# Kernel optimization log

Measured on AMD Instinct MI355X. Metric: run time of the kernel, lower is better.

Reference implementation:

```python
import jax, jax.numpy as jnp
import numpy as np

N_NODES = 50000
N_EDGES = 800000
IN_FEATS = 128
H_FEATS = 32
HEADS = 4
OUT_FEATS = 32
OUT_HEADS = 1
NEG_SLOPE = 0.2


def setup_inputs() -> dict:
    key = jax.random.key(0)
    ks = jax.random.split(key, 20)
    s = 0.05
    return {
        "features": jax.random.normal(ks[0], (N_NODES, IN_FEATS), jnp.float32),
        "src": jax.random.randint(ks[1], (N_EDGES,), 0, N_NODES, jnp.int32),
        "dst": jax.random.randint(ks[2], (N_EDGES,), 0, N_NODES, jnp.int32),
        "Ws0": jax.random.normal(ks[3], (IN_FEATS, HEADS * H_FEATS), jnp.float32) * s,
        "bs0": jnp.zeros((HEADS * H_FEATS,), jnp.float32),
        "Wd0": jax.random.normal(ks[4], (IN_FEATS, HEADS * H_FEATS), jnp.float32) * s,
        "bd0": jnp.zeros((HEADS * H_FEATS,), jnp.float32),
        "a0": jax.random.normal(ks[5], (HEADS, H_FEATS), jnp.float32) * s,
        "Ws1": jax.random.normal(ks[6], (HEADS * H_FEATS, HEADS * H_FEATS), jnp.float32) * s,
        "bs1": jnp.zeros((HEADS * H_FEATS,), jnp.float32),
        "Wd1": jax.random.normal(ks[7], (HEADS * H_FEATS, HEADS * H_FEATS), jnp.float32) * s,
        "bd1": jnp.zeros((HEADS * H_FEATS,), jnp.float32),
        "a1": jax.random.normal(ks[8], (HEADS, H_FEATS), jnp.float32) * s,
        "Ws2": jax.random.normal(ks[9], (HEADS * H_FEATS, OUT_HEADS * OUT_FEATS), jnp.float32) * s,
        "bs2": jnp.zeros((OUT_HEADS * OUT_FEATS,), jnp.float32),
        "Wd2": jax.random.normal(ks[10], (HEADS * H_FEATS, OUT_HEADS * OUT_FEATS), jnp.float32) * s,
        "bd2": jnp.zeros((OUT_HEADS * OUT_FEATS,), jnp.float32),
        "a2": jax.random.normal(ks[11], (OUT_HEADS, OUT_FEATS), jnp.float32) * s,
    }


def gatv2_conv(x, src, dst, Ws, bs, Wd, bd, attn, n_nodes):
    """DGL GATv2Conv (share_weights=False, residual=False, no dropout)."""
    heads, f = attn.shape
    feat_src = (x @ Ws + bs).reshape(-1, heads, f)  # [N, H, F]
    feat_dst = (x @ Wd + bd).reshape(-1, heads, f)  # [N, H, F]
    # per-edge GATv2 score: LeakyReLU(Wsrc h_u + Wdst h_v) . a
    e = jax.nn.leaky_relu(feat_src[src] + feat_dst[dst], NEG_SLOPE)  # [E, H, F]
    logits = jnp.einsum("ehf,hf->eh", e, attn)  # [E, H]
    # edge softmax over incoming edges of each dst node
    m = jax.ops.segment_max(logits, dst, num_segments=n_nodes)  # [N, H]
    ex = jnp.exp(logits - m[dst])
    denom = jax.ops.segment_sum(ex, dst, num_segments=n_nodes)  # [N, H]
    alpha = ex / denom[dst]  # [E, H]
    # scatter-aggregate messages
    msg = feat_src[src] * alpha[..., None]  # [E, H, F]
    return jax.ops.segment_sum(msg, dst, num_segments=n_nodes)  # [N, H, F]


def reference(features, src, dst,
              Ws0, bs0, Wd0, bd0, a0,
              Ws1, bs1, Wd1, bd1, a1,
              Ws2, bs2, Wd2, bd2, a2):
    n = features.shape[0]
    h = gatv2_conv(features, src, dst, Ws0, bs0, Wd0, bd0, a0, n)
    h = jax.nn.relu(h.reshape(n, -1))
    h = gatv2_conv(h, src, dst, Ws1, bs1, Wd1, bd1, a1, n)
    h = jax.nn.relu(h.reshape(n, -1))
    h = gatv2_conv(h, src, dst, Ws2, bs2, Wd2, bd2, a2, n)
    return h.mean(axis=1)  # [N, OUT_FEATS]
```

## Files before the change

### kernel.cpp

```cpp
#include <hip/hip_runtime.h>

typedef __attribute__((ext_vector_type(8))) short bf16x8;
typedef __attribute__((ext_vector_type(4))) float f32x4;

#define LOG2E 1.4426950408889634f

#define BINSH 8
#define NBIN 196
#define CHUNK 4096
#define K4CAP 6144

__device__ __forceinline__ unsigned bf_rn(float f) {
    unsigned u = __float_as_uint(f);
    u += 0x7fffu + ((u >> 16) & 1u);
    return u >> 16;
}
__device__ __forceinline__ float bf_lo(unsigned u) { return __uint_as_float(u << 16); }
__device__ __forceinline__ float bf_hi(unsigned u) { return __uint_as_float(u & 0xffff0000u); }

template <int CTRL>
__device__ __forceinline__ float dpp_radd(float x) {
    int t = __builtin_amdgcn_update_dpp(0, __float_as_int(x), CTRL, 0xF, 0xF, true);
    return x + __int_as_float(t);
}
__device__ __forceinline__ float sum8(float p) {
    p = dpp_radd<0x141>(p);
    p = dpp_radd<0x1B>(p);
    p = dpp_radd<0xB1>(p);
    return p;
}
__device__ __forceinline__ float dpp_swap1(float x) {
    return __int_as_float(__builtin_amdgcn_update_dpp(0, __float_as_int(x), 0xB1, 0xF, 0xF, true));
}

__device__ __forceinline__ float fast_exp2(float x) {
#if __has_builtin(__builtin_amdgcn_exp2f)
    return __builtin_amdgcn_exp2f(x);
#else
    return __expf(x * 0.6931471805599453f);
#endif
}


__global__ __launch_bounds__(256) void prep(
    const float* __restrict__ x, unsigned short* __restrict__ xb, int n4,
    const float* __restrict__ Ws0, const float* __restrict__ Wd0,
    const float* __restrict__ Ws1, const float* __restrict__ Wd1,
    const float* __restrict__ Ws2, const float* __restrict__ Wd2,
    unsigned short* __restrict__ wt0, unsigned short* __restrict__ wt1,
    unsigned short* __restrict__ wt2, int* __restrict__ binCnt,
    int* __restrict__ binOff) {
    int gid = blockIdx.x * blockDim.x + threadIdx.x;
    if (gid < NBIN) { binCnt[gid] = 0; binOff[gid] = 0; }
    if (gid < n4) {
        float4 v = *(const float4*)(x + (size_t)gid * 4);
        ushort4 r;
        r.x = (unsigned short)bf_rn(v.x); r.y = (unsigned short)bf_rn(v.y);
        r.z = (unsigned short)bf_rn(v.z); r.w = (unsigned short)bf_rn(v.w);
        *(ushort4*)(xb + (size_t)gid * 4) = r;
    } else {
        int g = gid - n4;
        if (g < 65536) {
            int l = g >> 15, loc = g & 32767;
            int c = loc >> 7, k = loc & 127;
            const float* W = (c < 128) ? (l ? Ws1 : Ws0) : (l ? Wd1 : Wd0);
            int cc = c & 127;
            float v = W[(size_t)k * 128 + cc];
            (l ? wt1 : wt0)[loc] = (unsigned short)bf_rn(v);
        } else if (g < 65536 + 8192) {
            int loc = g - 65536;
            int c = loc >> 7, k = loc & 127;
            const float* W = (c < 32) ? Ws2 : Wd2;
            int cc = (c < 32) ? c : c - 32;
            float v = W[(size_t)k * 32 + cc];
            wt2[loc] = (unsigned short)bf_rn(v);
        }
    }
}


template <int COLS2>
__device__ __forceinline__ void gemm_core(
    const unsigned short* __restrict__ xb, const unsigned short* __restrict__ wt,
    const float* __restrict__ bs, const float* __restrict__ bd,
    unsigned short* __restrict__ fs, unsigned short* __restrict__ fd,
    int n, int nch, int gwid, int nwaves) {
    constexpr int C  = COLS2 / 2;
    constexpr int NC = COLS2 / 64;

    const int lane = threadIdx.x & 63;
    const int m = lane & 15, quad = lane >> 4;
    const int cs = gwid % NC;
    const int cstride = nwaves / NC;

    float biasv[4];
#pragma unroll
    for (int ct = 0; ct < 4; ++ct) {
        int col = cs * 64 + ct * 16 + m;
        biasv[ct] = (col < C) ? bs[col] : bd[col - C];
    }

    for (int chunk = gwid / NC; chunk < nch; chunk += cstride) {
        const size_t r0 = (size_t)chunk * 64;

        f32x4 acc[4][4];
#pragma unroll
        for (int rt = 0; rt < 4; ++rt)
#pragma unroll
            for (int ct = 0; ct < 4; ++ct) acc[rt][ct] = (f32x4){0.f, 0.f, 0.f, 0.f};

#pragma unroll
        for (int ks = 0; ks < 4; ++ks) {
            const int ko = ks * 32 + quad * 8;
            bf16x8 a[4], b[4];
#pragma unroll
            for (int rt = 0; rt < 4; ++rt)
                a[rt] = *(const bf16x8*)(xb + (r0 + rt * 16 + m) * 128 + ko);
#pragma unroll
            for (int ct = 0; ct < 4; ++ct)
                b[ct] = *(const bf16x8*)(wt + (size_t)(cs * 64 + ct * 16 + m) * 128 + ko);
#pragma unroll
            for (int rt = 0; rt < 4; ++rt)
#pragma unroll
                for (int ct = 0; ct < 4; ++ct)
                    acc[rt][ct] = __builtin_amdgcn_mfma_f32_16x16x32_bf16(a[rt], b[ct], acc[rt][ct], 0, 0, 0);
        }

        const int odd = m & 1;
#pragma unroll
        for (int ct = 0; ct < 4; ++ct) {
            int colE = cs * 64 + ct * 16 + (m & ~1);
            unsigned short* ptr = (colE < C) ? fs : fd;
            int cc = (colE < C) ? colE : colE - C;
#pragma unroll
            for (int rt = 0; rt < 4; ++rt) {
                float v0 = acc[rt][ct][0] + biasv[ct];
                float v1 = acc[rt][ct][1] + biasv[ct];
                float v2 = acc[rt][ct][2] + biasv[ct];
                float v3 = acc[rt][ct][3] + biasv[ct];
                float s0 = dpp_swap1(v0), s1 = dpp_swap1(v1);
                float s2 = dpp_swap1(v2), s3 = dpp_swap1(v3);
                float aLo = odd ? s2 : v0, aHi = odd ? v2 : s0;
                float bLo = odd ? s3 : v1, bHi = odd ? v3 : s1;
                int rowA = (int)r0 + rt * 16 + quad * 4 + (odd ? 2 : 0);
                unsigned pa = (bf_rn(aHi) << 16) | bf_rn(aLo);
                unsigned pb = (bf_rn(bHi) << 16) | bf_rn(bLo);
                if (rowA < n)     *(unsigned*)(ptr + (size_t)rowA * C + cc)       = pa;
                if (rowA + 1 < n) *(unsigned*)(ptr + ((size_t)rowA + 1) * C + cc) = pb;
            }
        }
    }
}

template <int COLS2>
__global__ __launch_bounds__(256) void gemm_dual2(
    const unsigned short* __restrict__ xb, const unsigned short* __restrict__ wt,
    const float* __restrict__ bs, const float* __restrict__ bd,
    unsigned short* __restrict__ fs, unsigned short* __restrict__ fd,
    int n, int nch) {
    gemm_core<COLS2>(xb, wt, bs, bd, fs, fd, n, nch,
                     blockIdx.x * 4 + (threadIdx.x >> 6), gridDim.x * 4);
}


__global__ __launch_bounds__(256) void count_gemm0(
    const int* __restrict__ dst, int* __restrict__ binCnt, int e, int nchunks,
    const unsigned short* __restrict__ xb, const unsigned short* __restrict__ wt,
    const float* __restrict__ bs, const float* __restrict__ bd,
    unsigned short* __restrict__ fs, unsigned short* __restrict__ fd,
    int n, int nch) {
    if ((int)blockIdx.x < nchunks) {
        __shared__ int hist[NBIN];
        for (int t = threadIdx.x; t < NBIN; t += 256) hist[t] = 0;
        __syncthreads();
        int base = blockIdx.x * CHUNK;
        int cnt = min(CHUNK, e - base);
        for (int j = threadIdx.x; j < cnt; j += 256)
            atomicAdd(&hist[dst[base + j] >> BINSH], 1);
        __syncthreads();
        for (int t = threadIdx.x; t < NBIN; t += 256)
            if (hist[t]) atomicAdd(&binCnt[t], hist[t]);
    } else {
        int bid = blockIdx.x - nchunks;
        gemm_core<256>(xb, wt, bs, bd, fs, fd, n, nch,
                       bid * 4 + (threadIdx.x >> 6), (gridDim.x - nchunks) * 4);
    }
}


__global__ __launch_bounds__(256) void bin_scatter(
    const int* __restrict__ src, const int* __restrict__ dst,
    const int* __restrict__ binCnt, int* __restrict__ binOff,
    unsigned* __restrict__ ebin, int e) {
    __shared__ int hist[256];
    __shared__ int seg[256];
    __shared__ int bbase[256];
    __shared__ int gbase[NBIN];
    __shared__ unsigned pack[CHUNK];
    for (int t = threadIdx.x; t < 256; t += 256) hist[t] = 0;
    if (threadIdx.x < 64) {
        int l = threadIdx.x;
        int s = 0, loc[4];
#pragma unroll
        for (int k = 0; k < 4; ++k) {
            int idx = l * 4 + k;
            int v = (idx < NBIN) ? binCnt[idx] : 0;
            loc[k] = s; s += v;
        }
        int incl = s;
        for (int off = 1; off < 64; off <<= 1) {
            int tt = __shfl_up(incl, off);
            if (l >= off) incl += tt;
        }
        int excl = incl - s;
#pragma unroll
        for (int k = 0; k < 4; ++k) bbase[l * 4 + k] = excl + loc[k];
    }
    __syncthreads();
    int base = blockIdx.x * CHUNK;
    int cnt = min(CHUNK, e - base);

    for (int j = threadIdx.x; j < cnt; j += 256)
        atomicAdd(&hist[dst[base + j] >> BINSH], 1);
    __syncthreads();
    if (threadIdx.x < 64) {
        int l = threadIdx.x;
        int s = 0, loc[4];
#pragma unroll
        for (int k = 0; k < 4; ++k) { loc[k] = s; s += hist[l * 4 + k]; }
        int incl = s;
        for (int off = 1; off < 64; off <<= 1) {
            int tt = __shfl_up(incl, off);
            if (l >= off) incl += tt;
        }
        int excl = incl - s;
#pragma unroll
        for (int k = 0; k < 4; ++k) seg[l * 4 + k] = excl + loc[k];
    }
    __syncthreads();
    if (threadIdx.x < NBIN && hist[threadIdx.x])
        gbase[threadIdx.x] = bbase[threadIdx.x] + atomicAdd(&binOff[threadIdx.x], hist[threadIdx.x]);
    __syncthreads();
    for (int t = threadIdx.x; t < 256; t += 256) hist[t] = seg[t];
    __syncthreads();
    for (int j = threadIdx.x; j < cnt; j += 256) {
        int d = dst[base + j], s = src[base + j];
        int b = d >> BINSH, dl = d & ((1 << BINSH) - 1);
        int pos = atomicAdd(&hist[b], 1);
        pack[pos] = ((unsigned)b << 24) | ((unsigned)dl << 16) | (unsigned)s;
    }
    __syncthreads();
    for (int j = threadIdx.x; j < cnt; j += 256) {
        unsigned wv = pack[j];
        int b = wv >> 24;
        ebin[gbase[b] + (j - seg[b])] = wv;
    }
}


__global__ __launch_bounds__(256) void csr_build(
    const unsigned* __restrict__ ebin, const int* __restrict__ binCnt,
    int* __restrict__ rowp, int* __restrict__ csrc, int n) {
    __shared__ int hist[256];
    __shared__ int seg[256];
    __shared__ int bbase[257];
    __shared__ unsigned stage[K4CAP];
    int b = blockIdx.x;
    if (threadIdx.x < 64) {
        int l = threadIdx.x;
        int s = 0, loc[4];
#pragma unroll
        for (int k = 0; k < 4; ++k) {
            int idx = l * 4 + k;
            int v = (idx < NBIN) ? binCnt[idx] : 0;
            loc[k] = s; s += v;
        }
        int incl = s;
        for (int off = 1; off < 64; off <<= 1) {
            int tt = __shfl_up(incl, off);
            if (l >= off) incl += tt;
        }
        int excl = incl - s;
#pragma unroll
        for (int k = 0; k < 4; ++k) bbase[l * 4 + k] = excl + loc[k];
        if (l == 63) bbase[256] = incl;
    }
    for (int t = threadIdx.x; t < 256; t += 256) hist[t] = 0;
    __syncthreads();
    int e0 = bbase[b], e1 = bbase[b + 1];
    int n0 = b << BINSH;
    int nn = min(256, n - n0);
    if (b == NBIN - 1 && threadIdx.x == 0) rowp[n] = bbase[NBIN];
    for (int i = e0 + threadIdx.x; i < e1; i += 256) {
        unsigned wv = ebin[i];
        atomicAdd(&hist[(wv >> 16) & 255], 1);
        int off = i - e0;
        if (off < K4CAP) stage[off] = wv;
    }
    __syncthreads();
    if (threadIdx.x < 64) {
        int l = threadIdx.x;
        int s = 0, loc[4];
#pragma unroll
        for (int k = 0; k < 4; ++k) { loc[k] = s; s += hist[l * 4 + k]; }
        int incl = s;
        for (int off = 1; off < 64; off <<= 1) {
            int tt = __shfl_up(incl, off);
            if (l >= off) incl += tt;
        }
        int excl = incl - s;
#pragma unroll
        for (int k = 0; k < 4; ++k) seg[l * 4 + k] = excl + loc[k];
    }
    __syncthreads();
    for (int t = threadIdx.x; t < nn; t += 256) rowp[n0 + t] = e0 + seg[t];
    for (int t = threadIdx.x; t < 256; t += 256) hist[t] = seg[t];
    __syncthreads();
    for (int i = e0 + threadIdx.x; i < e1; i += 256) {
        int off = i - e0;
        unsigned wv = (off < K4CAP) ? stage[off] : ebin[i];
        int dl = (wv >> 16) & 255;
        int pos = e0 + atomicAdd(&hist[dl], 1);
        csrc[pos] = (int)(wv & 0xFFFFu);
    }
}


#define EDGE_BODY(u, mval)                                          \
    do {                                                            \
        float x0 = bf_lo((u).x), x1 = bf_hi((u).x);                 \
        float x2 = bf_lo((u).y), x3 = bf_hi((u).y);                 \
        float t0 = x0 + fd0, t1 = x1 + fd1;                         \
        float t2 = x2 + fd2, t3 = x3 + fd3;                         \
        float p = a060 * t0;                                        \
        p = fmaf(a040, fabsf(t0), p);                               \
        p = fmaf(a061, t1, p); p = fmaf(a041, fabsf(t1), p);        \
        p = fmaf(a062, t2, p); p = fmaf(a042, fabsf(t2), p);        \
        p = fmaf(a063, t3, p); p = fmaf(a043, fabsf(t3), p);        \
        p = sum8(p);                                                \
        float ex = fast_exp2(p) * (mval);                           \
        denom += ex;                                                \
        acc0 = fmaf(ex, x0, acc0); acc1 = fmaf(ex, x1, acc1);       \
        acc2 = fmaf(ex, x2, acc2); acc3 = fmaf(ex, x3, acc3);       \
    } while (0)

__global__ __launch_bounds__(256) void conv128(
    const unsigned short* __restrict__ fs, const unsigned short* __restrict__ fd,
    const float* __restrict__ attn, const int* __restrict__ rowp,
    const int* __restrict__ csrc, unsigned short* __restrict__ out, int n) {
    const int nwaves = gridDim.x * 4;
    const int wid0 = blockIdx.x * 4 + (threadIdx.x >> 6);
    const int lane = threadIdx.x & 63;
    const int half = lane >> 5;
    const int q = lane & 31;

    float4 av = *(const float4*)(attn + q * 4);
    const float a060 = av.x * 0.6f * LOG2E, a040 = av.x * 0.4f * LOG2E;
    const float a061 = av.y * 0.6f * LOG2E, a041 = av.y * 0.4f * LOG2E;
    const float a062 = av.z * 0.6f * LOG2E, a042 = av.z * 0.4f * LOG2E;
    const float a063 = av.w * 0.6f * LOG2E, a043 = av.w * 0.4f * LOG2E;

    for (int wid = wid0; wid < n; wid += nwaves) {
        uint2 ud = *(const uint2*)(fd + (size_t)wid * 128 + q * 4);
        float fd0 = bf_lo(ud.x), fd1 = bf_hi(ud.x);
        float fd2 = bf_lo(ud.y), fd3 = bf_hi(ud.y);
        int rs = rowp[wid], re = rowp[wid + 1];
        float acc0 = 0.f, acc1 = 0.f, acc2 = 0.f, acc3 = 0.f, denom = 0.f;

        int i = rs;
        for (; i + 3 < re; i += 4) {
            int sA = csrc[i + half];
            int sB = csrc[i + 2 + half];
            uint2 uA = *(const uint2*)(fs + ((size_t)sA << 7) + q * 4);
            uint2 uB = *(const uint2*)(fs + ((size_t)sB << 7) + q * 4);
            EDGE_BODY(uA, 1.0f);
            EDGE_BODY(uB, 1.0f);
        }
        for (; i + 1 < re; i += 2) {
            int s = csrc[i + half];
            uint2 u = *(const uint2*)(fs + ((size_t)s << 7) + q * 4);
            EDGE_BODY(u, 1.0f);
        }
        if (i < re) {
            int s = csrc[i];
            uint2 u = *(const uint2*)(fs + ((size_t)s << 7) + q * 4);
            float mval = half ? 0.f : 1.f;
            EDGE_BODY(u, mval);
        }
        acc0 += __shfl_xor(acc0, 32); acc1 += __shfl_xor(acc1, 32);
        acc2 += __shfl_xor(acc2, 32); acc3 += __shfl_xor(acc3, 32);
        denom += __shfl_xor(denom, 32);
        float inv = (re > rs) ? 1.f / denom : 0.f;
        float r0 = fmaxf(acc0 * inv, 0.f), r1 = fmaxf(acc1 * inv, 0.f);
        float r2 = fmaxf(acc2 * inv, 0.f), r3 = fmaxf(acc3 * inv, 0.f);
        if (half == 0) {
            uint2 o;
            o.x = (bf_rn(r1) << 16) | bf_rn(r0);
            o.y = (bf_rn(r3) << 16) | bf_rn(r2);
            ((uint2*)(out + (size_t)wid * 128))[q] = o;
        }
    }
}

__global__ __launch_bounds__(256) void conv32(
    const unsigned short* __restrict__ fs, const unsigned short* __restrict__ fd,
    const float* __restrict__ attn, const int* __restrict__ rowp,
    const int* __restrict__ csrc, float* __restrict__ out, int n) {
    const int nwaves = gridDim.x * 4;
    const int wid0 = blockIdx.x * 4 + (threadIdx.x >> 6);
    const int lane = threadIdx.x & 63;
    const int g = lane >> 3;
    const int c = lane & 7;

    float4 av = *(const float4*)(attn + c * 4);
    const float a060 = av.x * 0.6f * LOG2E, a040 = av.x * 0.4f * LOG2E;
    const float a061 = av.y * 0.6f * LOG2E, a041 = av.y * 0.4f * LOG2E;
    const float a062 = av.z * 0.6f * LOG2E, a042 = av.z * 0.4f * LOG2E;
    const float a063 = av.w * 0.6f * LOG2E, a043 = av.w * 0.4f * LOG2E;

    for (int wid = wid0; wid < n; wid += nwaves) {
        uint2 ud = *(const uint2*)(fd + (size_t)wid * 32 + c * 4);
        float fd0 = bf_lo(ud.x), fd1 = bf_hi(ud.x);
        float fd2 = bf_lo(ud.y), fd3 = bf_hi(ud.y);
        int rs = rowp[wid], re = rowp[wid + 1];
        float acc0 = 0.f, acc1 = 0.f, acc2 = 0.f, acc3 = 0.f, denom = 0.f;

        int i = rs;
        for (; i + 7 < re; i += 8) {
            int s = csrc[i + g];
            uint2 u = *(const uint2*)(fs + ((size_t)s << 5) + c * 4);
            EDGE_BODY(u, 1.0f);
        }
        if (i < re) {
            int idx = i + g;
            int s = csrc[min(idx, re - 1)];
            uint2 u = *(const uint2*)(fs + ((size_t)s << 5) + c * 4);
            float mval = (idx < re) ? 1.f : 0.f;
            EDGE_BODY(u, mval);
        }
        acc0 = dpp_radd<0x128>(acc0); acc1 = dpp_radd<0x128>(acc1);
        acc2 = dpp_radd<0x128>(acc2); acc3 = dpp_radd<0x128>(acc3);
        denom = dpp_radd<0x128>(denom);
        acc0 += __shfl_xor(acc0, 16); acc1 += __shfl_xor(acc1, 16);
        acc2 += __shfl_xor(acc2, 16); acc3 += __shfl_xor(acc3, 16);
        denom += __shfl_xor(denom, 16);
        acc0 += __shfl_xor(acc0, 32); acc1 += __shfl_xor(acc1, 32);
        acc2 += __shfl_xor(acc2, 32); acc3 += __shfl_xor(acc3, 32);
        denom += __shfl_xor(denom, 32);
        float inv = (re > rs) ? 1.f / denom : 0.f;
        if (lane < 8) {
            float4 o;
            o.x = acc0 * inv; o.y = acc1 * inv;
            o.z = acc2 * inv; o.w = acc3 * inv;
            *(float4*)(out + (size_t)wid * 32 + c * 4) = o;
        }
    }
}


extern "C" void kernel_launch(void* const* d_in, const int* in_sizes, int n_in,
                              void* d_out, int out_size, void* d_ws, size_t ws_size,
                              hipStream_t stream) {
    const float* feats = (const float*)d_in[0];
    const int*   src   = (const int*)d_in[1];
    const int*   dst   = (const int*)d_in[2];
    const float* Ws0 = (const float*)d_in[3],  *bs0 = (const float*)d_in[4];
    const float* Wd0 = (const float*)d_in[5],  *bd0 = (const float*)d_in[6];
    const float* a0  = (const float*)d_in[7];
    const float* Ws1 = (const float*)d_in[8],  *bs1 = (const float*)d_in[9];
    const float* Wd1 = (const float*)d_in[10], *bd1 = (const float*)d_in[11];
    const float* a1  = (const float*)d_in[12];
    const float* Ws2 = (const float*)d_in[13], *bs2 = (const float*)d_in[14];
    const float* Wd2 = (const float*)d_in[15], *bd2 = (const float*)d_in[16];
    const float* a2  = (const float*)d_in[17];

    const int N = in_sizes[0] / 128;
    const int E = in_sizes[1];
    const int nch = (N + 63) / 64;
    const int NPAD = nch * 64;

    char* ws = (char*)d_ws;
    const size_t featB = (size_t)NPAD * 128 * 2;
    unsigned short* xb  = (unsigned short*)(ws);
    unsigned short* hb  = (unsigned short*)(ws + featB);
    unsigned short* fsb = (unsigned short*)(ws + 2 * featB);
    unsigned short* fdb = (unsigned short*)(ws + 3 * featB);
    char* p = ws + 4 * featB;
    unsigned short* wt0 = (unsigned short*)p; p += 256 * 128 * 2;
    unsigned short* wt1 = (unsigned short*)p; p += 256 * 128 * 2;
    unsigned short* wt2 = (unsigned short*)p; p += 64 * 128 * 2;
    int* rowp    = (int*)p;      p += ((size_t)(N + 1) * 4 + 255) / 256 * 256;
    int* binCnt  = (int*)p;      p += (NBIN * 4 + 255) / 256 * 256;
    int* binOff  = (int*)p;      p += (NBIN * 4 + 255) / 256 * 256;
    unsigned* ebin = (unsigned*)p; p += (size_t)E * 4;
    int* csrc    = (int*)p;

    const int nchunks = (E + CHUNK - 1) / CHUNK;
    const int n4 = N * 128 / 4;

    const int g256 = nch;
    const int g64  = (nch + 3) / 4;
    const int convGrid = 2048;

    prep<<<(n4 + 73728 + 255) / 256, 256, 0, stream>>>(
        feats, xb, n4, Ws0, Wd0, Ws1, Wd1, Ws2, Wd2, wt0, wt1, wt2, binCnt, binOff);

    count_gemm0<<<nchunks + g256, 256, 0, stream>>>(
        dst, binCnt, E, nchunks, xb, wt0, bs0, bd0, fsb, fdb, N, nch);

    bin_scatter<<<nchunks, 256, 0, stream>>>(src, dst, binCnt, binOff, ebin, E);
    csr_build<<<NBIN, 256, 0, stream>>>(ebin, binCnt, rowp, csrc, N);

    conv128<<<convGrid, 256, 0, stream>>>(fsb, fdb, a0, rowp, csrc, hb, N);
    gemm_dual2<256><<<g256, 256, 0, stream>>>(hb, wt1, bs1, bd1, fsb, fdb, N, nch);
    conv128<<<convGrid, 256, 0, stream>>>(fsb, fdb, a1, rowp, csrc, hb, N);
    gemm_dual2<64><<<g64, 256, 0, stream>>>(hb, wt2, bs2, bd2, fsb, fdb, N, nch);
    conv32<<<convGrid, 256, 0, stream>>>(fsb, fdb, a2, rowp, csrc, (float*)d_out, N);
}
```

Baseline: 282.4 us.

## Balance conv work across waves by edge count using binary search over rowp

Adds a small kernel that binary-searches the CSR row pointer to give each of the 8192 conv waves a contiguous node range with about the same number of edges. The three conv kernels then walk their assigned contiguous range instead of grid-striding over nodes. This targets load imbalance from the varying in-degree and gives more sequential access to rowp and csrc, at the cost of an extra launch. With random uniform dst, degrees are roughly Poisson, so the imbalance under the old striding was already small.

```diff
diff --git a/kernel.cpp b/kernel.cpp
--- a/kernel.cpp
+++ b/kernel.cpp
@@ -326,6 +326,21 @@
 }
 
 
+__global__ void balance(const int* __restrict__ rowp, int* __restrict__ wstart,
+                        int n, int e, int nw) {
+    int w = blockIdx.x * blockDim.x + threadIdx.x;
+    if (w > nw) return;
+    if (w == nw) { wstart[nw] = n; return; }
+    int target = (int)(((long long)e * w) / nw);
+    int lo = 0, hi = n;
+    while (lo < hi) {
+        int mid = (lo + hi) >> 1;
+        if (rowp[mid] < target) lo = mid + 1; else hi = mid;
+    }
+    wstart[w] = lo;
+}
+
+
 #define EDGE_BODY(u, mval)                                          \
     do {                                                            \
         float x0 = bf_lo((u).x), x1 = bf_hi((u).x);                 \
@@ -347,9 +362,9 @@
 __global__ __launch_bounds__(256) void conv128(
     const unsigned short* __restrict__ fs, const unsigned short* __restrict__ fd,
     const float* __restrict__ attn, const int* __restrict__ rowp,
-    const int* __restrict__ csrc, unsigned short* __restrict__ out, int n) {
-    const int nwaves = gridDim.x * 4;
-    const int wid0 = blockIdx.x * 4 + (threadIdx.x >> 6);
+    const int* __restrict__ csrc, const int* __restrict__ wstart,
+    unsigned short* __restrict__ out, int n) {
+    const int w = blockIdx.x * 4 + (threadIdx.x >> 6);
     const int lane = threadIdx.x & 63;
     const int half = lane >> 5;
     const int q = lane & 31;
@@ -360,7 +375,9 @@
     const float a062 = av.z * 0.6f * LOG2E, a042 = av.z * 0.4f * LOG2E;
     const float a063 = av.w * 0.6f * LOG2E, a043 = av.w * 0.4f * LOG2E;
 
-    for (int wid = wid0; wid < n; wid += nwaves) {
+    const int row0 = wstart[w], row1 = wstart[w + 1];
+
+    for (int wid = row0; wid < row1; ++wid) {
         uint2 ud = *(const uint2*)(fd + (size_t)wid * 128 + q * 4);
         float fd0 = bf_lo(ud.x), fd1 = bf_hi(ud.x);
         float fd2 = bf_lo(ud.y), fd3 = bf_hi(ud.y);
@@ -405,9 +422,9 @@
 __global__ __launch_bounds__(256) void conv32(
     const unsigned short* __restrict__ fs, const unsigned short* __restrict__ fd,
     const float* __restrict__ attn, const int* __restrict__ rowp,
-    const int* __restrict__ csrc, float* __restrict__ out, int n) {
-    const int nwaves = gridDim.x * 4;
-    const int wid0 = blockIdx.x * 4 + (threadIdx.x >> 6);
+    const int* __restrict__ csrc, const int* __restrict__ wstart,
+    float* __restrict__ out, int n) {
+    const int w = blockIdx.x * 4 + (threadIdx.x >> 6);
     const int lane = threadIdx.x & 63;
     const int g = lane >> 3;
     const int c = lane & 7;
@@ -418,7 +435,9 @@
     const float a062 = av.z * 0.6f * LOG2E, a042 = av.z * 0.4f * LOG2E;
     const float a063 = av.w * 0.6f * LOG2E, a043 = av.w * 0.4f * LOG2E;
 
-    for (int wid = wid0; wid < n; wid += nwaves) {
+    const int row0 = wstart[w], row1 = wstart[w + 1];
+
+    for (int wid = row0; wid < row1; ++wid) {
         uint2 ud = *(const uint2*)(fd + (size_t)wid * 32 + c * 4);
         float fd0 = bf_lo(ud.x), fd1 = bf_hi(ud.x);
         float fd2 = bf_lo(ud.y), fd3 = bf_hi(ud.y);
@@ -492,6 +511,7 @@
     int* rowp    = (int*)p;      p += ((size_t)(N + 1) * 4 + 255) / 256 * 256;
     int* binCnt  = (int*)p;      p += (NBIN * 4 + 255) / 256 * 256;
     int* binOff  = (int*)p;      p += (NBIN * 4 + 255) / 256 * 256;
+    int* wstart  = (int*)p;      p += ((size_t)(8192 + 1) * 4 + 255) / 256 * 256;
     unsigned* ebin = (unsigned*)p; p += (size_t)E * 4;
     int* csrc    = (int*)p;
 
@@ -501,6 +521,7 @@
     const int g256 = nch;
     const int g64  = (nch + 3) / 4;
     const int convGrid = 2048;
+    const int NW = convGrid * 4;
 
     prep<<<(n4 + 73728 + 255) / 256, 256, 0, stream>>>(
         feats, xb, n4, Ws0, Wd0, Ws1, Wd1, Ws2, Wd2, wt0, wt1, wt2, binCnt, binOff);
@@ -511,9 +532,11 @@
     bin_scatter<<<nchunks, 256, 0, stream>>>(src, dst, binCnt, binOff, ebin, E);
     csr_build<<<NBIN, 256, 0, stream>>>(ebin, binCnt, rowp, csrc, N);
 
-    conv128<<<convGrid, 256, 0, stream>>>(fsb, fdb, a0, rowp, csrc, hb, N);
+    balance<<<(NW + 1 + 255) / 256, 256, 0, stream>>>(rowp, wstart, N, E, NW);
+
+    conv128<<<convGrid, 256, 0, stream>>>(fsb, fdb, a0, rowp, csrc, wstart, hb, N);
     gemm_dual2<256><<<g256, 256, 0, stream>>>(hb, wt1, bs1, bd1, fsb, fdb, N, nch);
-    conv128<<<convGrid, 256, 0, stream>>>(fsb, fdb, a1, rowp, csrc, hb, N);
+    conv128<<<convGrid, 256, 0, stream>>>(fsb, fdb, a1, rowp, csrc, wstart, hb, N);
     gemm_dual2<64><<<g64, 256, 0, stream>>>(hb, wt2, bs2, bd2, fsb, fdb, N, nch);
-    conv32<<<convGrid, 256, 0, stream>>>(fsb, fdb, a2, rowp, csrc, (float*)d_out, N);
-}
+    conv32<<<convGrid, 256, 0, stream>>>(fsb, fdb, a2, rowp, csrc, wstart, (float*)d_out, N);
+}
```

Result: slower. 289.2 us (+2.4%).
